# Kernel tuning notes

Measured on AMD Instinct MI355X. Metric: run time of the kernel, lower is better.

Reference implementation:

```python
import jax, jax.numpy as jnp
import numpy as np

N = 40000          # nodes
E = 640000         # edges (avg degree 16)
D_MODEL = 128
H = 8              # num_heads
DH = 16            # d_head
DFF = 512
CLAMP = 5.0
EPS = 1e-5


def setup_inputs() -> dict:
    key = jax.random.key(0)
    ks = jax.random.split(key, 10)
    s = 0.08  # weight init scale
    return {
        "feat": jax.random.normal(ks[0], (N, D_MODEL), dtype=jnp.float32),
        "src": jax.random.randint(ks[1], (E,), 0, N, dtype=jnp.int32),
        "dst": jax.random.randint(ks[2], (E,), 0, N, dtype=jnp.int32),
        "Wq": jax.random.normal(ks[3], (H * DH, D_MODEL), dtype=jnp.float32) * s,
        "Wk": jax.random.normal(ks[4], (H * DH, D_MODEL), dtype=jnp.float32) * s,
        "Wv": jax.random.normal(ks[5], (H * DH, D_MODEL), dtype=jnp.float32) * s,
        "Wo": jax.random.normal(ks[6], (D_MODEL, H * DH), dtype=jnp.float32) * s,
        "ln1_g": jnp.ones((D_MODEL,), jnp.float32),
        "ln1_b": jnp.zeros((D_MODEL,), jnp.float32),
        "W1": jax.random.normal(ks[7], (DFF, D_MODEL), dtype=jnp.float32) * s,
        "b1": jnp.zeros((DFF,), jnp.float32),
        "W2": jax.random.normal(ks[8], (D_MODEL, DFF), dtype=jnp.float32) * s,
        "b2": jnp.zeros((D_MODEL,), jnp.float32),
        "ln2_g": jnp.ones((D_MODEL,), jnp.float32),
        "ln2_b": jnp.zeros((D_MODEL,), jnp.float32),
    }


def _layer_norm(x, g, b):
    mu = jnp.mean(x, axis=-1, keepdims=True)
    var = jnp.mean(jnp.square(x - mu), axis=-1, keepdims=True)
    return (x - mu) * jax.lax.rsqrt(var + EPS) * g + b


def reference(feat, src, dst, Wq, Wk, Wv, Wo, ln1_g, ln1_b, W1, b1, W2, b2, ln2_g, ln2_b):
    n = feat.shape[0]
    # Node-level projections (equivalent to DGL's per-edge Linear on gathered feats)
    q = (feat @ Wq.T).reshape(n, H, DH)
    k = (feat @ Wk.T).reshape(n, H, DH)
    v = (feat @ Wv.T).reshape(n, H, DH)

    # Per-edge multi-head attention logits: q[dst] . k[src] / sqrt(d_head), clamped
    u = jnp.sum(q[dst] * k[src], axis=-1) / np.sqrt(DH)   # [E, H]
    u = jnp.clip(u, -CLAMP, CLAMP)

    # Ragged edge-softmax over incoming edges of each dst node
    m = jax.ops.segment_max(u, dst, num_segments=n)        # [N, H]
    e = jnp.exp(u - m[dst])                                # [E, H]
    denom = jax.ops.segment_sum(e, dst, num_segments=n)    # [N, H]
    a = e / denom[dst]                                     # [E, H]

    # Weighted V scatter-reduce back to dst nodes
    av = (a[:, :, None] * v[src]).reshape(-1, H * DH)      # [E, H*DH]
    sum_av = jax.ops.segment_sum(av, dst, num_segments=n)  # [N, H*DH]
    uh = sum_av @ Wo.T                                     # [N, d_model]

    h1 = _layer_norm(feat + uh, ln1_g, ln1_b)
    ffn = jax.nn.relu(h1 @ W1.T + b1) @ W2.T + b2
    return _layer_norm(h1 + ffn, ln2_g, ln2_b)
```

## Files before the change

### kernel.cpp

```cpp
#include <hip/hip_runtime.h>

#define DM 128
#define DFF 512
#define CLAMP_V 5.0f
#define LN_EPS 1e-5f

typedef __attribute__((ext_vector_type(8))) short bf16x8;
typedef __attribute__((ext_vector_type(4))) float f32x4;

__device__ __forceinline__ float b2f(ushort u) {
  union { uint u; float f; } x; x.u = ((uint)u) << 16; return x.f;
}
__device__ __forceinline__ ushort f2b(float f) {
  union { float f; uint u; } x; x.f = f;
  uint r = x.u + 0x7FFFu + ((x.u >> 16) & 1u);
  return (ushort)(r >> 16);
}
__device__ __forceinline__ void unpackw(uint w, float& lo, float& hi) {
  union { uint u; float f; } A, B;
  A.u = w << 16; B.u = w & 0xFFFF0000u;
  lo = A.f; hi = B.f;
}
__device__ __forceinline__ void unpack8w(uint4 w, float* o) {
  unpackw(w.x, o[0], o[1]); unpackw(w.y, o[2], o[3]);
  unpackw(w.z, o[4], o[5]); unpackw(w.w, o[6], o[7]);
}

__global__ void k_cast(const float* __restrict__ s, ushort* __restrict__ d, int n) {
  int i4 = (blockIdx.x * blockDim.x + threadIdx.x) * 4;
  if (i4 + 3 < n) {
    float4 v = *reinterpret_cast<const float4*>(s + i4);
    ushort4 o; o.x = f2b(v.x); o.y = f2b(v.y); o.z = f2b(v.z); o.w = f2b(v.w);
    *reinterpret_cast<ushort4*>(d + i4) = o;
  } else {
    for (; i4 < n; ++i4) d[i4] = f2b(s[i4]);
  }
}

__global__ void k_castw(const float* __restrict__ wq, const float* __restrict__ wk,
                        const float* __restrict__ wv, const float* __restrict__ wo,
                        const float* __restrict__ w1, const float* __restrict__ w2,
                        ushort* __restrict__ d) {
  int i4 = (blockIdx.x * blockDim.x + threadIdx.x) * 4;
  if (i4 >= 196608) return;
  const float* s; int o;
  if      (i4 < 16384)  { s = wq; o = i4; }
  else if (i4 < 32768)  { s = wk; o = i4 - 16384; }
  else if (i4 < 49152)  { s = wv; o = i4 - 32768; }
  else if (i4 < 65536)  { s = wo; o = i4 - 49152; }
  else if (i4 < 131072) { s = w1; o = i4 - 65536; }
  else                  { s = w2; o = i4 - 131072; }
  float4 v = *reinterpret_cast<const float4*>(s + o);
  ushort4 u; u.x = f2b(v.x); u.y = f2b(v.y); u.z = f2b(v.z); u.w = f2b(v.w);
  *reinterpret_cast<ushort4*>(d + i4) = u;
}

__global__ void k_count(const int* __restrict__ dst, int* __restrict__ deg, int E) {
  int e = blockIdx.x * blockDim.x + threadIdx.x;
  if (e < E) atomicAdd(&deg[dst[e]], 1);
}

#define SC_EPB 1024

__global__ __launch_bounds__(256) void k_scan1(const int* __restrict__ deg,
                                               int* __restrict__ off,
                                               int* __restrict__ bsum, int n) {
  __shared__ int sh[256];
  const int t = threadIdx.x;
  int base = blockIdx.x * SC_EPB + t * 4;
  int4 v = {0, 0, 0, 0};
  if (base + 3 < n) {
    v = *reinterpret_cast<const int4*>(deg + base);
  } else {
    if (base     < n) v.x = deg[base];
    if (base + 1 < n) v.y = deg[base + 1];
    if (base + 2 < n) v.z = deg[base + 2];
    if (base + 3 < n) v.w = deg[base + 3];
  }
  int s = v.x + v.y + v.z + v.w;
  sh[t] = s;
  __syncthreads();
  #pragma unroll
  for (int d = 1; d < 256; d <<= 1) {
    int x = 0;
    if (t >= d) x = sh[t - d];
    __syncthreads();
    sh[t] += x;
    __syncthreads();
  }
  int ex = sh[t] - s;
  if (base + 3 < n) {
    int4 o; o.x = ex; o.y = ex + v.x; o.z = ex + v.x + v.y; o.w = ex + v.x + v.y + v.z;
    *reinterpret_cast<int4*>(off + base) = o;
  } else {
    if (base     < n) off[base]     = ex;
    if (base + 1 < n) off[base + 1] = ex + v.x;
    if (base + 2 < n) off[base + 2] = ex + v.x + v.y;
    if (base + 3 < n) off[base + 3] = ex + v.x + v.y + v.z;
  }
  if (t == 255) bsum[blockIdx.x] = sh[255];
}

__global__ __launch_bounds__(256) void k_scan2(int* __restrict__ bsum, int nb) {
  __shared__ int sh[256];
  const int t = threadIdx.x;
  int v = (t < nb) ? bsum[t] : 0;
  sh[t] = v;
  __syncthreads();
  #pragma unroll
  for (int d = 1; d < 256; d <<= 1) {
    int x = 0;
    if (t >= d) x = sh[t - d];
    __syncthreads();
    sh[t] += x;
    __syncthreads();
  }
  if (t < nb) bsum[t] = sh[t] - v;
}

__global__ __launch_bounds__(256) void k_scan3(int* __restrict__ off,
                                               const int* __restrict__ bsum,
                                               int n, int E) {
  int add = bsum[blockIdx.x];
  int base = blockIdx.x * SC_EPB + threadIdx.x * 4;
  if (base + 3 < n) {
    int4 v = *reinterpret_cast<int4*>(off + base);
    v.x += add; v.y += add; v.z += add; v.w += add;
    *reinterpret_cast<int4*>(off + base) = v;
  } else {
    if (base     < n) off[base]     += add;
    if (base + 1 < n) off[base + 1] += add;
    if (base + 2 < n) off[base + 2] += add;
  }
  if (blockIdx.x == 0 && threadIdx.x == 0) off[n] = E;
}

__global__ void k_scatter(const int* __restrict__ src, const int* __restrict__ dst,
                          const int* __restrict__ off, int* __restrict__ cur,
                          int* __restrict__ csr, int E) {
  int e = blockIdx.x * blockDim.x + threadIdx.x;
  if (e < E) {
    int d = dst[e];
    int p = off[d] + atomicAdd(&cur[d], 1);
    csr[p] = src[e];
  }
}

#define BM 128
#define BN 128
#define BK 64

template<int FLAGS, bool OUTF, bool OUTB>
__global__ __launch_bounds__(256, 3) void k_mm(
    const ushort* __restrict__ A, const ushort* __restrict__ W,
    const float* __restrict__ bias, const float* __restrict__ res,
    const float* __restrict__ lng, const float* __restrict__ lnbv,
    float* __restrict__ Cf, ushort* __restrict__ Cb,
    int M, int NO, int K)
{
  __shared__ ushort As[BM * BK];
  __shared__ ushort Ws[BN * BK];
  __shared__ float lnred[(FLAGS & 8) ? 512 : 4];

  const int tid = threadIdx.x;
  const int wv = tid >> 6, ln = tid & 63;
  const int bm = blockIdx.y * BM, bn = blockIdx.x * BN;
  const int wrow = (wv >> 1) * 64, wcol = (wv & 1) * 64;

  f32x4 acc[4][4] = {};
  const int o_base = wv * 1024 + ln * 16;

  for (int k0 = 0; k0 < K; k0 += BK) {
    #pragma unroll
    for (int is = 0; is < 4; ++is) {
      int o = is * 4096 + o_base;
      int row = o >> 7;
      int c = ((o >> 4) & 7) ^ (row & 7);
      int gm = bm + row; if (gm >= M) gm = M - 1;
      const ushort* srcA = A + (size_t)gm * K + k0 + c * 8;
      __builtin_amdgcn_global_load_lds(
          (const __attribute__((address_space(1))) void*)srcA,
          (__attribute__((address_space(3))) void*)((char*)As + is * 4096 + wv * 1024),
          16, 0, 0);
      int gn = bn + row;
      const ushort* srcW = W + (size_t)gn * K + k0 + c * 8;
      __builtin_amdgcn_global_load_lds(
          (const __attribute__((address_space(1))) void*)srcW,
          (__attribute__((address_space(3))) void*)((char*)Ws + is * 4096 + wv * 1024),
          16, 0, 0);
    }
    __syncthreads();

    const char* AsB = (const char*)As;
    const char* WsB = (const char*)Ws;
    #pragma unroll
    for (int kk = 0; kk < 2; ++kk) {
      bf16x8 af[4], bf[4];
      #pragma unroll
      for (int m = 0; m < 4; ++m) {
        int r = wrow + m * 16 + (ln & 15);
        int c = kk * 4 + (ln >> 4);
        af[m] = *reinterpret_cast<const bf16x8*>(AsB + r * 128 + ((c ^ (r & 7)) << 4));
      }
      #pragma unroll
      for (int n = 0; n < 4; ++n) {
        int r = wcol + n * 16 + (ln & 15);
        int c = kk * 4 + (ln >> 4);
        bf[n] = *reinterpret_cast<const bf16x8*>(WsB + r * 128 + ((c ^ (r & 7)) << 4));
      }
      #pragma unroll
      for (int m = 0; m < 4; ++m)
        #pragma unroll
        for (int n = 0; n < 4; ++n)
          acc[m][n] = __builtin_amdgcn_mfma_f32_16x16x32_bf16(af[m], bf[n], acc[m][n], 0, 0, 0);
    }
    __syncthreads();
  }

  if constexpr ((FLAGS & 8) != 0) {
    #pragma unroll
    for (int m = 0; m < 4; ++m)
      #pragma unroll
      for (int n = 0; n < 4; ++n) {
        int gc = wcol + n * 16 + (ln & 15);
        float bsv = (FLAGS & 1) ? bias[gc] : 0.f;
        #pragma unroll
        for (int r = 0; r < 4; ++r) {
          int gr = bm + wrow + m * 16 + (ln >> 4) * 4 + r;
          float v = acc[m][n][r] + bsv;
          if (FLAGS & 2) v = fmaxf(v, 0.f);
          if (FLAGS & 4) v += res[(size_t)min(gr, M - 1) * 128 + gc];
          acc[m][n][r] = v;
        }
      }
    #pragma unroll
    for (int m = 0; m < 4; ++m)
      #pragma unroll
      for (int r = 0; r < 4; ++r) {
        float sm = acc[m][0][r] + acc[m][1][r] + acc[m][2][r] + acc[m][3][r];
        float sq = acc[m][0][r] * acc[m][0][r] + acc[m][1][r] * acc[m][1][r]
                 + acc[m][2][r] * acc[m][2][r] + acc[m][3][r] * acc[m][3][r];
        #pragma unroll
        for (int msk = 1; msk <= 8; msk <<= 1) {
          sm += __shfl_xor(sm, msk);
          sq += __shfl_xor(sq, msk);
        }
        if ((ln & 15) == 0) {
          int row = wrow + m * 16 + (ln >> 4) * 4 + r;
          lnred[row * 4 + (wv & 1) * 2]     = sm;
          lnred[row * 4 + (wv & 1) * 2 + 1] = sq;
        }
      }
    __syncthreads();
    #pragma unroll
    for (int m = 0; m < 4; ++m)
      #pragma unroll
      for (int r = 0; r < 4; ++r) {
        int row = wrow + m * 16 + (ln >> 4) * 4 + r;
        int gr = bm + row;
        float sm = lnred[row * 4] + lnred[row * 4 + 2];
        float sq = lnred[row * 4 + 1] + lnred[row * 4 + 3];
        float mu = sm * (1.f / 128.f);
        float var = fmaxf(sq * (1.f / 128.f) - mu * mu, 0.f);
        float rstd = rsqrtf(var + LN_EPS);
        if (gr < M) {
          #pragma unroll
          for (int n = 0; n < 4; ++n) {
            int gc = wcol + n * 16 + (ln & 15);
            float y = (acc[m][n][r] - mu) * rstd * lng[gc] + lnbv[gc];
            if (OUTF) Cf[(size_t)gr * 128 + gc] = y;
            if (OUTB) Cb[(size_t)gr * 128 + gc] = f2b(y);
          }
        }
      }
  } else {
    #pragma unroll
    for (int m = 0; m < 4; ++m) {
      int gr0 = bm + wrow + m * 16 + (ln >> 4) * 4;
      #pragma unroll
      for (int n = 0; n < 4; ++n) {
        int gc = bn + wcol + n * 16 + (ln & 15);
        float bsv = (FLAGS & 1) ? bias[gc] : 0.f;
        #pragma unroll
        for (int r = 0; r < 4; ++r) {
          int gr = gr0 + r;
          if (gr >= M) continue;
          float v = acc[m][n][r] + bsv;
          if (FLAGS & 2) v = fmaxf(v, 0.f);
          if (FLAGS & 4) v += res[(size_t)gr * NO + gc];
          if (OUTF) Cf[(size_t)gr * NO + gc] = v;
          if (OUTB) Cb[(size_t)gr * NO + gc] = f2b(v);
        }
      }
    }
  }
}

__global__ __launch_bounds__(256) void k_attn(
    const ushort* __restrict__ q, const ushort* __restrict__ kv,
    const int* __restrict__ off, const int* __restrict__ csr,
    ushort* __restrict__ sav, int n)
{
  int node = blockIdx.x * 4 + (threadIdx.x >> 6);
  int lane = threadIdx.x & 63;
  if (node >= n) return;
  const int g = lane >> 3, sl = lane & 7;

  const ushort* qr = q + (size_t)node * 128 + sl * 16;
  uint4 qw0 = *reinterpret_cast<const uint4*>(qr);
  uint4 qw1 = *reinterpret_cast<const uint4*>(qr + 8);
  float qv[16];
  unpack8w(qw0, qv); unpack8w(qw1, qv + 8);

  int b = off[node], e = off[node + 1];
  float m = -1e30f, s = 0.f;
  float a[16] = {};
  int nIt = (e - b + 7) >> 3;
  int idx = b + g;
  int sn = (b < e) ? csr[min(idx, e - 1)] : 0;

  for (int i = 0; i < nIt; ++i) {
    bool act = idx < e;
    const ushort* kr = kv + (size_t)sn * 256 + sl * 16;
    uint4 kw0 = *reinterpret_cast<const uint4*>(kr);
    uint4 kw1 = *reinterpret_cast<const uint4*>(kr + 8);
    uint4 vw0 = *reinterpret_cast<const uint4*>(kr + 128);
    uint4 vw1 = *reinterpret_cast<const uint4*>(kr + 136);
    idx += 8;
    if (i + 1 < nIt) sn = csr[min(idx, e - 1)];

    float kk[16];
    unpack8w(kw0, kk); unpack8w(kw1, kk + 8);
    float p = 0.f;
    #pragma unroll
    for (int j = 0; j < 16; ++j) p = fmaf(qv[j], kk[j], p);
    float u = fminf(fmaxf(p * 0.25f, -CLAMP_V), CLAMP_V);
    if (act) {
      float mn = fmaxf(m, u);
      float f = __expf(m - mn);
      float w = __expf(u - mn);
      s = s * f + w;
      float vvv[16];
      unpack8w(vw0, vvv); unpack8w(vw1, vvv + 8);
      #pragma unroll
      for (int j = 0; j < 16; ++j) a[j] = a[j] * f + w * vvv[j];
      m = mn;
    }
  }

  #pragma unroll
  for (int msk = 8; msk <= 32; msk <<= 1) {
    float mo = __shfl_xor(m, msk);
    float so = __shfl_xor(s, msk);
    float ao[16];
    #pragma unroll
    for (int j = 0; j < 16; ++j) ao[j] = __shfl_xor(a[j], msk);
    float mn = fmaxf(m, mo);
    float f1 = __expf(m - mn), f2 = __expf(mo - mn);
    s = s * f1 + so * f2;
    #pragma unroll
    for (int j = 0; j < 16; ++j) a[j] = a[j] * f1 + ao[j] * f2;
    m = mn;
  }

  float inv = (s > 0.f) ? 1.f / s : 0.f;
  if (g == 0) {
    uint w[8];
    #pragma unroll
    for (int j = 0; j < 8; ++j)
      w[j] = (uint)f2b(a[2 * j] * inv) | ((uint)f2b(a[2 * j + 1] * inv) << 16);
    ushort* outp = sav + (size_t)node * 128 + sl * 16;
    uint4 o0 = {w[0], w[1], w[2], w[3]};
    uint4 o1 = {w[4], w[5], w[6], w[7]};
    *reinterpret_cast<uint4*>(outp) = o0;
    *reinterpret_cast<uint4*>(outp + 8) = o1;
  }
}

extern "C" void kernel_launch(void* const* d_in, const int* in_sizes, int n_in,
                              void* d_out, int out_size, void* d_ws, size_t ws_size,
                              hipStream_t stream)
{
  const float* feat = (const float*)d_in[0];
  const int*   src  = (const int*)d_in[1];
  const int*   dst  = (const int*)d_in[2];
  const float* Wq   = (const float*)d_in[3];
  const float* Wk   = (const float*)d_in[4];
  const float* Wv   = (const float*)d_in[5];
  const float* Wo   = (const float*)d_in[6];
  const float* ln1g = (const float*)d_in[7];
  const float* ln1b = (const float*)d_in[8];
  const float* W1   = (const float*)d_in[9];
  const float* b1   = (const float*)d_in[10];
  const float* W2   = (const float*)d_in[11];
  const float* b2   = (const float*)d_in[12];
  const float* ln2g = (const float*)d_in[13];
  const float* ln2b = (const float*)d_in[14];
  float* out = (float*)d_out;

  const int N = in_sizes[0] / DM;
  const int E = in_sizes[1];
  const size_t NB = (size_t)N;

  char* wsb = (char*)d_ws;
  ushort* q_bf    = (ushort*)wsb;
  ushort* kv_bf   = (ushort*)(wsb + NB * 256);
  ushort* sav_bf  = (ushort*)(wsb + NB * 768);
  ushort* mid_bf  = (ushort*)wsb;
  float*  h1      = (float*)(wsb + NB * 1024);
  ushort* h1b     = (ushort*)(wsb + NB * 1536);
  ushort* feat_bf = (ushort*)(wsb + NB * 1792);
  ushort* wbf     = (ushort*)(wsb + NB * 2048);
  ushort* wqkv_bf = wbf;
  ushort* wo_bf   = wbf + 49152;
  ushort* w1_bf   = wbf + 65536;
  ushort* w2_bf   = wbf + 131072;
  int* ib  = (int*)(wbf + 196608);
  int* deg = ib;
  int* cur = ib + N;
  int* off = ib + 2 * N;
  int* csr = ib + 3 * N + 1;
  int* bsum = csr + E;

  hipMemsetAsync(deg, 0, 2 * (size_t)N * sizeof(int), stream);

  int nf = N * DM;
  k_cast<<<(nf / 4 + 255) / 256, 256, 0, stream>>>(feat, feat_bf, nf);
  k_castw<<<192, 256, 0, stream>>>(Wq, Wk, Wv, Wo, W1, W2, wbf);

  int eb = (E + 255) / 256;
  int nbk = (N + SC_EPB - 1) / SC_EPB;
  k_count<<<eb, 256, 0, stream>>>(dst, deg, E);
  k_scan1<<<nbk, 256, 0, stream>>>(deg, off, bsum, N);
  k_scan2<<<1, 256, 0, stream>>>(bsum, nbk);
  k_scan3<<<nbk, 256, 0, stream>>>(off, bsum, N, E);
  k_scatter<<<eb, 256, 0, stream>>>(src, dst, off, cur, csr, E);

  const int gy = (N + BM - 1) / BM;
  int nb4 = (N + 3) / 4;

  k_mm<0, false, true><<<dim3(1, gy), 256, 0, stream>>>(
      feat_bf, wqkv_bf, nullptr, nullptr, nullptr, nullptr, nullptr, q_bf, N, DM, DM);
  k_mm<0, false, true><<<dim3(2, gy), 256, 0, stream>>>(
      feat_bf, wqkv_bf + 16384, nullptr, nullptr, nullptr, nullptr, nullptr, kv_bf, N, 256, DM);

  k_attn<<<nb4, 256, 0, stream>>>(q_bf, kv_bf, off, csr, sav_bf, N);

  k_mm<4 | 8, true, true><<<dim3(1, gy), 256, 0, stream>>>(
      sav_bf, wo_bf, nullptr, feat, ln1g, ln1b, h1, h1b, N, DM, DM);

  k_mm<1 | 2, false, true><<<dim3(4, gy), 256, 0, stream>>>(
      h1b, w1_bf, b1, nullptr, nullptr, nullptr, nullptr, mid_bf, N, DFF, DM);

  k_mm<1 | 4 | 8, true, false><<<dim3(1, gy), 256, 0, stream>>>(
      mid_bf, w2_bf, b2, h1, ln2g, ln2b, out, nullptr, N, DM, DFF);
}
```

Before: 203.5 us.

## Add persistent weight-stationary GEMMs, double-buffer K loop, drop online softmax max

Adds a persistent 512-thread GEMM (k_mmS) for the K=128 projections. It keeps one 128x128 weight tile resident in LDS, walks several row tiles per block, and double-buffers the A tiles. It also fuses the Q and KV projections into one launch. The K=512 FFN-down GEMM now double-buffers its K loop at lower occupancy. The attention kernel drops the running max and uses the fixed clamp bound 5 as the softmax shift, removing rescale exps and branches. That shift is exact in math because logits are clamped, but it loses the per-node max normalization.

```diff
diff --git a/kernel.cpp b/kernel.cpp
--- a/kernel.cpp
+++ b/kernel.cpp
@@ -146,56 +146,240 @@
   }
 }
 
+template<int FLAGS, bool QKVSPLIT, bool OUTF, bool OUTB>
+__global__ __launch_bounds__(512, 1) void k_mmS(
+    const ushort* __restrict__ A, const ushort* __restrict__ W,
+    const float* __restrict__ bias, const float* __restrict__ res,
+    const float* __restrict__ lng, const float* __restrict__ lnbv,
+    float* __restrict__ Cf, ushort* __restrict__ Cb, ushort* __restrict__ Cb2,
+    int M, int ldc)
+{
+  __shared__ ushort Bs[128 * 128];
+  __shared__ ushort As[2][128 * 128];
+  __shared__ float lnred[(FLAGS & 8) ? 1024 : 4];
+
+  const int tid = threadIdx.x;
+  const int wv = tid >> 6, ln = tid & 63;
+  const int bnb = blockIdx.x;
+  const int wrow = (wv >> 2) * 64, wcol = (wv & 3) * 32;
+  const int o_base = wv * 1024 + ln * 16;
+
+  const int nT = (M + 127) >> 7;
+  const int T = (nT + gridDim.y - 1) / gridDim.y;
+  const int t0 = blockIdx.y * T;
+  const int t1 = min(t0 + T, nT);
+  if (t0 >= nT) return;
+
+  #pragma unroll
+  for (int is = 0; is < 4; ++is) {
+    int o = is * 8192 + o_base;
+    int row = o >> 8;
+    int c = ((o >> 4) & 15) ^ (row & 15);
+    const ushort* s = W + (size_t)(bnb * 128 + row) * 128 + c * 8;
+    __builtin_amdgcn_global_load_lds(
+        (const __attribute__((address_space(1))) void*)s,
+        (__attribute__((address_space(3))) void*)((char*)Bs + is * 8192 + wv * 1024),
+        16, 0, 0);
+  }
+  {
+    #pragma unroll
+    for (int is = 0; is < 4; ++is) {
+      int o = is * 8192 + o_base;
+      int row = o >> 8;
+      int c = ((o >> 4) & 15) ^ (row & 15);
+      int gr = min(t0 * 128 + row, M - 1);
+      const ushort* s = A + (size_t)gr * 128 + c * 8;
+      __builtin_amdgcn_global_load_lds(
+          (const __attribute__((address_space(1))) void*)s,
+          (__attribute__((address_space(3))) void*)((char*)As[0] + is * 8192 + wv * 1024),
+          16, 0, 0);
+    }
+  }
+  __syncthreads();
+
+  int buf = 0;
+  for (int t = t0; t < t1; ++t) {
+    if (t + 1 < t1) {
+      #pragma unroll
+      for (int is = 0; is < 4; ++is) {
+        int o = is * 8192 + o_base;
+        int row = o >> 8;
+        int c = ((o >> 4) & 15) ^ (row & 15);
+        int gr = min((t + 1) * 128 + row, M - 1);
+        const ushort* s = A + (size_t)gr * 128 + c * 8;
+        __builtin_amdgcn_global_load_lds(
+            (const __attribute__((address_space(1))) void*)s,
+            (__attribute__((address_space(3))) void*)((char*)As[buf ^ 1] + is * 8192 + wv * 1024),
+            16, 0, 0);
+      }
+    }
+
+    f32x4 acc[4][2] = {};
+    const char* AsB = (const char*)As[buf];
+    const char* BsB = (const char*)Bs;
+    #pragma unroll
+    for (int kk = 0; kk < 4; ++kk) {
+      bf16x8 af[4], bfr[2];
+      #pragma unroll
+      for (int m = 0; m < 4; ++m) {
+        int r = wrow + m * 16 + (ln & 15);
+        int c = kk * 4 + (ln >> 4);
+        af[m] = *reinterpret_cast<const bf16x8*>(AsB + r * 256 + ((c ^ (r & 15)) << 4));
+      }
+      #pragma unroll
+      for (int n = 0; n < 2; ++n) {
+        int r = wcol + n * 16 + (ln & 15);
+        int c = kk * 4 + (ln >> 4);
+        bfr[n] = *reinterpret_cast<const bf16x8*>(BsB + r * 256 + ((c ^ (r & 15)) << 4));
+      }
+      #pragma unroll
+      for (int m = 0; m < 4; ++m)
+        #pragma unroll
+        for (int n = 0; n < 2; ++n)
+          acc[m][n] = __builtin_amdgcn_mfma_f32_16x16x32_bf16(af[m], bfr[n], acc[m][n], 0, 0, 0);
+    }
+
+    const int mbase = t * 128;
+    if constexpr ((FLAGS & 8) != 0) {
+      #pragma unroll
+      for (int m = 0; m < 4; ++m)
+        #pragma unroll
+        for (int n = 0; n < 2; ++n) {
+          int gc = wcol + n * 16 + (ln & 15);
+          #pragma unroll
+          for (int r = 0; r < 4; ++r) {
+            int gr = mbase + wrow + m * 16 + (ln >> 4) * 4 + r;
+            float v = acc[m][n][r];
+            if (FLAGS & 1) v += bias[gc];
+            if (FLAGS & 2) v = fmaxf(v, 0.f);
+            if (FLAGS & 4) v += res[(size_t)min(gr, M - 1) * 128 + gc];
+            acc[m][n][r] = v;
+          }
+        }
+      #pragma unroll
+      for (int m = 0; m < 4; ++m)
+        #pragma unroll
+        for (int r = 0; r < 4; ++r) {
+          float sm = acc[m][0][r] + acc[m][1][r];
+          float sq = acc[m][0][r] * acc[m][0][r] + acc[m][1][r] * acc[m][1][r];
+          #pragma unroll
+          for (int msk = 1; msk <= 8; msk <<= 1) {
+            sm += __shfl_xor(sm, msk);
+            sq += __shfl_xor(sq, msk);
+          }
+          if ((ln & 15) == 0) {
+            int row = wrow + m * 16 + (ln >> 4) * 4 + r;
+            lnred[row * 8 + (wv & 3) * 2]     = sm;
+            lnred[row * 8 + (wv & 3) * 2 + 1] = sq;
+          }
+        }
+      __syncthreads();
+      #pragma unroll
+      for (int m = 0; m < 4; ++m)
+        #pragma unroll
+        for (int r = 0; r < 4; ++r) {
+          int row = wrow + m * 16 + (ln >> 4) * 4 + r;
+          int gr = mbase + row;
+          float sm = lnred[row * 8] + lnred[row * 8 + 2] + lnred[row * 8 + 4] + lnred[row * 8 + 6];
+          float sq = lnred[row * 8 + 1] + lnred[row * 8 + 3] + lnred[row * 8 + 5] + lnred[row * 8 + 7];
+          float mu = sm * (1.f / 128.f);
+          float var = fmaxf(sq * (1.f / 128.f) - mu * mu, 0.f);
+          float rstd = rsqrtf(var + LN_EPS);
+          if (gr < M) {
+            #pragma unroll
+            for (int n = 0; n < 2; ++n) {
+              int gc = wcol + n * 16 + (ln & 15);
+              float y = (acc[m][n][r] - mu) * rstd * lng[gc] + lnbv[gc];
+              if (OUTF) Cf[(size_t)gr * 128 + gc] = y;
+              if (OUTB) Cb[(size_t)gr * 128 + gc] = f2b(y);
+            }
+          }
+        }
+    } else {
+      #pragma unroll
+      for (int m = 0; m < 4; ++m) {
+        int gr0 = mbase + wrow + m * 16 + (ln >> 4) * 4;
+        #pragma unroll
+        for (int n = 0; n < 2; ++n) {
+          int gcl = wcol + n * 16 + (ln & 15);
+          float bsv = (FLAGS & 1) ? bias[bnb * 128 + gcl] : 0.f;
+          #pragma unroll
+          for (int r = 0; r < 4; ++r) {
+            int gr = gr0 + r;
+            if (gr >= M) continue;
+            float v = acc[m][n][r] + bsv;
+            if (FLAGS & 2) v = fmaxf(v, 0.f);
+            if (QKVSPLIT) {
+              if (bnb == 0) Cb[(size_t)gr * 128 + gcl] = f2b(v);
+              else          Cb2[(size_t)gr * 256 + (bnb - 1) * 128 + gcl] = f2b(v);
+            } else {
+              if (OUTF) Cf[(size_t)gr * ldc + bnb * 128 + gcl] = v;
+              if (OUTB) Cb[(size_t)gr * ldc + bnb * 128 + gcl] = f2b(v);
+            }
+          }
+        }
+      }
+    }
+    __syncthreads();
+    buf ^= 1;
+  }
+}
+
 #define BM 128
 #define BN 128
 #define BK 64
 
 template<int FLAGS, bool OUTF, bool OUTB>
-__global__ __launch_bounds__(256, 3) void k_mm(
+__global__ __launch_bounds__(256, 2) void k_mm2(
     const ushort* __restrict__ A, const ushort* __restrict__ W,
     const float* __restrict__ bias, const float* __restrict__ res,
     const float* __restrict__ lng, const float* __restrict__ lnbv,
     float* __restrict__ Cf, ushort* __restrict__ Cb,
     int M, int NO, int K)
 {
-  __shared__ ushort As[BM * BK];
-  __shared__ ushort Ws[BN * BK];
+  __shared__ ushort As[2][BM * BK];
+  __shared__ ushort Ws[2][BN * BK];
   __shared__ float lnred[(FLAGS & 8) ? 512 : 4];
 
   const int tid = threadIdx.x;
   const int wv = tid >> 6, ln = tid & 63;
   const int bm = blockIdx.y * BM, bn = blockIdx.x * BN;
   const int wrow = (wv >> 1) * 64, wcol = (wv & 1) * 64;
-
-  f32x4 acc[4][4] = {};
   const int o_base = wv * 1024 + ln * 16;
 
-  for (int k0 = 0; k0 < K; k0 += BK) {
+  auto STG = [&](int kidx, int b) {
     #pragma unroll
     for (int is = 0; is < 4; ++is) {
       int o = is * 4096 + o_base;
       int row = o >> 7;
       int c = ((o >> 4) & 7) ^ (row & 7);
-      int gm = bm + row; if (gm >= M) gm = M - 1;
-      const ushort* srcA = A + (size_t)gm * K + k0 + c * 8;
+      int gm = min(bm + row, M - 1);
+      const ushort* sA = A + (size_t)gm * K + kidx * BK + c * 8;
       __builtin_amdgcn_global_load_lds(
-          (const __attribute__((address_space(1))) void*)srcA,
-          (__attribute__((address_space(3))) void*)((char*)As + is * 4096 + wv * 1024),
+          (const __attribute__((address_space(1))) void*)sA,
+          (__attribute__((address_space(3))) void*)((char*)As[b] + is * 4096 + wv * 1024),
           16, 0, 0);
       int gn = bn + row;
-      const ushort* srcW = W + (size_t)gn * K + k0 + c * 8;
+      const ushort* sW = W + (size_t)gn * K + kidx * BK + c * 8;
       __builtin_amdgcn_global_load_lds(
-          (const __attribute__((address_space(1))) void*)srcW,
-          (__attribute__((address_space(3))) void*)((char*)Ws + is * 4096 + wv * 1024),
+          (const __attribute__((address_space(1))) void*)sW,
+          (__attribute__((address_space(3))) void*)((char*)Ws[b] + is * 4096 + wv * 1024),
           16, 0, 0);
     }
-    __syncthreads();
-
-    const char* AsB = (const char*)As;
-    const char* WsB = (const char*)Ws;
+  };
+
+  f32x4 acc[4][4] = {};
+  const int KT = K >> 6;
+  STG(0, 0);
+  __syncthreads();
+  int buf = 0;
+  for (int i = 0; i < KT; ++i) {
+    if (i + 1 < KT) STG(i + 1, buf ^ 1);
+    const char* AsB = (const char*)As[buf];
+    const char* WsB = (const char*)Ws[buf];
     #pragma unroll
     for (int kk = 0; kk < 2; ++kk) {
-      bf16x8 af[4], bf[4];
+      bf16x8 af[4], bfr[4];
       #pragma unroll
       for (int m = 0; m < 4; ++m) {
         int r = wrow + m * 16 + (ln & 15);
@@ -206,15 +390,16 @@
       for (int n = 0; n < 4; ++n) {
         int r = wcol + n * 16 + (ln & 15);
         int c = kk * 4 + (ln >> 4);
-        bf[n] = *reinterpret_cast<const bf16x8*>(WsB + r * 128 + ((c ^ (r & 7)) << 4));
+        bfr[n] = *reinterpret_cast<const bf16x8*>(WsB + r * 128 + ((c ^ (r & 7)) << 4));
       }
       #pragma unroll
       for (int m = 0; m < 4; ++m)
         #pragma unroll
         for (int n = 0; n < 4; ++n)
-          acc[m][n] = __builtin_amdgcn_mfma_f32_16x16x32_bf16(af[m], bf[n], acc[m][n], 0, 0, 0);
+          acc[m][n] = __builtin_amdgcn_mfma_f32_16x16x32_bf16(af[m], bfr[n], acc[m][n], 0, 0, 0);
     }
     __syncthreads();
+    buf ^= 1;
   }
 
   if constexpr ((FLAGS & 8) != 0) {
@@ -313,7 +498,7 @@
   unpack8w(qw0, qv); unpack8w(qw1, qv + 8);
 
   int b = off[node], e = off[node + 1];
-  float m = -1e30f, s = 0.f;
+  float s = 0.f;
   float a[16] = {};
   int nIt = (e - b + 7) >> 3;
   int idx = b + g;
@@ -335,32 +520,20 @@
     #pragma unroll
     for (int j = 0; j < 16; ++j) p = fmaf(qv[j], kk[j], p);
     float u = fminf(fmaxf(p * 0.25f, -CLAMP_V), CLAMP_V);
-    if (act) {
-      float mn = fmaxf(m, u);
-      float f = __expf(m - mn);
-      float w = __expf(u - mn);
-      s = s * f + w;
-      float vvv[16];
-      unpack8w(vw0, vvv); unpack8w(vw1, vvv + 8);
-      #pragma unroll
-      for (int j = 0; j < 16; ++j) a[j] = a[j] * f + w * vvv[j];
-      m = mn;
-    }
+    float w = __expf(u - CLAMP_V);
+    w = act ? w : 0.f;
+    s += w;
+    float vvv[16];
+    unpack8w(vw0, vvv); unpack8w(vw1, vvv + 8);
+    #pragma unroll
+    for (int j = 0; j < 16; ++j) a[j] = fmaf(w, vvv[j], a[j]);
   }
 
   #pragma unroll
   for (int msk = 8; msk <= 32; msk <<= 1) {
-    float mo = __shfl_xor(m, msk);
-    float so = __shfl_xor(s, msk);
-    float ao[16];
-    #pragma unroll
-    for (int j = 0; j < 16; ++j) ao[j] = __shfl_xor(a[j], msk);
-    float mn = fmaxf(m, mo);
-    float f1 = __expf(m - mn), f2 = __expf(mo - mn);
-    s = s * f1 + so * f2;
-    #pragma unroll
-    for (int j = 0; j < 16; ++j) a[j] = a[j] * f1 + ao[j] * f2;
-    m = mn;
+    s += __shfl_xor(s, msk);
+    #pragma unroll
+    for (int j = 0; j < 16; ++j) a[j] += __shfl_xor(a[j], msk);
   }
 
   float inv = (s > 0.f) ? 1.f / s : 0.f;
@@ -436,22 +609,31 @@
   k_scan3<<<nbk, 256, 0, stream>>>(off, bsum, N, E);
   k_scatter<<<eb, 256, 0, stream>>>(src, dst, off, cur, csr, E);
 
-  const int gy = (N + BM - 1) / BM;
   int nb4 = (N + 3) / 4;
-
-  k_mm<0, false, true><<<dim3(1, gy), 256, 0, stream>>>(
-      feat_bf, wqkv_bf, nullptr, nullptr, nullptr, nullptr, nullptr, q_bf, N, DM, DM);
-  k_mm<0, false, true><<<dim3(2, gy), 256, 0, stream>>>(
-      feat_bf, wqkv_bf + 16384, nullptr, nullptr, nullptr, nullptr, nullptr, kv_bf, N, 256, DM);
+  const int nT = (N + 127) / 128;
+
+  {
+    int S = (nT + 3) / 4;
+    k_mmS<0, true, false, true><<<dim3(3, S), 512, 0, stream>>>(
+        feat_bf, wqkv_bf, nullptr, nullptr, nullptr, nullptr,
+        nullptr, q_bf, kv_bf, N, 0);
+  }
 
   k_attn<<<nb4, 256, 0, stream>>>(q_bf, kv_bf, off, csr, sav_bf, N);
 
-  k_mm<4 | 8, true, true><<<dim3(1, gy), 256, 0, stream>>>(
-      sav_bf, wo_bf, nullptr, feat, ln1g, ln1b, h1, h1b, N, DM, DM);
-
-  k_mm<1 | 2, false, true><<<dim3(4, gy), 256, 0, stream>>>(
-      h1b, w1_bf, b1, nullptr, nullptr, nullptr, nullptr, mid_bf, N, DFF, DM);
-
-  k_mm<1 | 4 | 8, true, false><<<dim3(1, gy), 256, 0, stream>>>(
+  {
+    int S = (nT + 1) / 2;
+    k_mmS<4 | 8, false, true, true><<<dim3(1, S), 512, 0, stream>>>(
+        sav_bf, wo_bf, nullptr, feat, ln1g, ln1b, h1, h1b, nullptr, N, 128);
+  }
+
+  {
+    int S = (nT + 4) / 5;
+    k_mmS<1 | 2, false, false, true><<<dim3(4, S), 512, 0, stream>>>(
+        h1b, w1_bf, b1, nullptr, nullptr, nullptr,
+        nullptr, mid_bf, nullptr, N, DFF);
+  }
+
+  k_mm2<1 | 4 | 8, true, false><<<dim3(1, nT), 256, 0, stream>>>(
       mid_bf, w2_bf, b2, h1, ln2g, ln2b, out, nullptr, N, DM, DFF);
 }
```

Result: no change. 199.9 us (-1.8%).

## Drop LDS staging in GEMMs, fixed-max softmax, and merge small launches

Applied to the files above, without the earlier changes.

The GEMM kernel now loads MFMA fragments straight from global memory instead of staging them through LDS, which removes the barriers but relies on cache for reuse. The Q and KV projections become one launch that writes two outputs. The attention kernel drops the online-softmax running max and uses the clamp bound as a fixed shift, which is exact in math because logits are clamped to 5. It also replaces the max-rescale reduction with plain sums. The two cast kernels are merged, and scan2 is folded into scan3 through a per-block wave reduction.

```diff
diff --git a/kernel.cpp b/kernel.cpp
--- a/kernel.cpp
+++ b/kernel.cpp
@@ -26,22 +26,20 @@
   unpackw(w.z, o[4], o[5]); unpackw(w.w, o[6], o[7]);
 }
 
-__global__ void k_cast(const float* __restrict__ s, ushort* __restrict__ d, int n) {
-  int i4 = (blockIdx.x * blockDim.x + threadIdx.x) * 4;
-  if (i4 + 3 < n) {
-    float4 v = *reinterpret_cast<const float4*>(s + i4);
+__global__ void k_castall(const float* __restrict__ feat,
+                          const float* __restrict__ wq, const float* __restrict__ wk,
+                          const float* __restrict__ wv, const float* __restrict__ wo,
+                          const float* __restrict__ w1, const float* __restrict__ w2,
+                          ushort* __restrict__ feat_bf, ushort* __restrict__ wbf,
+                          int nf4) {
+  int i = blockIdx.x * blockDim.x + threadIdx.x;
+  if (i < nf4) {
+    float4 v = *reinterpret_cast<const float4*>(feat + i * 4);
     ushort4 o; o.x = f2b(v.x); o.y = f2b(v.y); o.z = f2b(v.z); o.w = f2b(v.w);
-    *reinterpret_cast<ushort4*>(d + i4) = o;
-  } else {
-    for (; i4 < n; ++i4) d[i4] = f2b(s[i4]);
-  }
-}
-
-__global__ void k_castw(const float* __restrict__ wq, const float* __restrict__ wk,
-                        const float* __restrict__ wv, const float* __restrict__ wo,
-                        const float* __restrict__ w1, const float* __restrict__ w2,
-                        ushort* __restrict__ d) {
-  int i4 = (blockIdx.x * blockDim.x + threadIdx.x) * 4;
+    *reinterpret_cast<ushort4*>(feat_bf + i * 4) = o;
+    return;
+  }
+  int i4 = (i - nf4) * 4;
   if (i4 >= 196608) return;
   const float* s; int o;
   if      (i4 < 16384)  { s = wq; o = i4; }
@@ -52,7 +50,7 @@
   else                  { s = w2; o = i4 - 131072; }
   float4 v = *reinterpret_cast<const float4*>(s + o);
   ushort4 u; u.x = f2b(v.x); u.y = f2b(v.y); u.z = f2b(v.z); u.w = f2b(v.w);
-  *reinterpret_cast<ushort4*>(d + i4) = u;
+  *reinterpret_cast<ushort4*>(wbf + i4) = u;
 }
 
 __global__ void k_count(const int* __restrict__ dst, int* __restrict__ deg, int E) {
@@ -101,28 +99,20 @@
   if (t == 255) bsum[blockIdx.x] = sh[255];
 }
 
-__global__ __launch_bounds__(256) void k_scan2(int* __restrict__ bsum, int nb) {
-  __shared__ int sh[256];
-  const int t = threadIdx.x;
-  int v = (t < nb) ? bsum[t] : 0;
-  sh[t] = v;
-  __syncthreads();
-  #pragma unroll
-  for (int d = 1; d < 256; d <<= 1) {
-    int x = 0;
-    if (t >= d) x = sh[t - d];
-    __syncthreads();
-    sh[t] += x;
-    __syncthreads();
-  }
-  if (t < nb) bsum[t] = sh[t] - v;
-}
-
 __global__ __launch_bounds__(256) void k_scan3(int* __restrict__ off,
                                                const int* __restrict__ bsum,
-                                               int n, int E) {
-  int add = bsum[blockIdx.x];
-  int base = blockIdx.x * SC_EPB + threadIdx.x * 4;
+                                               int nbk, int n, int E) {
+  __shared__ int sadd;
+  const int t = threadIdx.x;
+  if (t < 64) {
+    int v = (t < nbk && t < (int)blockIdx.x) ? bsum[t] : 0;
+    #pragma unroll
+    for (int msk = 1; msk < 64; msk <<= 1) v += __shfl_xor(v, msk);
+    if (t == 0) sadd = v;
+  }
+  __syncthreads();
+  int add = sadd;
+  int base = blockIdx.x * SC_EPB + t * 4;
   if (base + 3 < n) {
     int4 v = *reinterpret_cast<int4*>(off + base);
     v.x += add; v.y += add; v.z += add; v.w += add;
@@ -132,7 +122,7 @@
     if (base + 1 < n) off[base + 1] += add;
     if (base + 2 < n) off[base + 2] += add;
   }
-  if (blockIdx.x == 0 && threadIdx.x == 0) off[n] = E;
+  if (blockIdx.x == 0 && t == 0) off[n] = E;
 }
 
 __global__ void k_scatter(const int* __restrict__ src, const int* __restrict__ dst,
@@ -146,75 +136,48 @@
   }
 }
 
-#define BM 128
-#define BN 128
-#define BK 64
-
-template<int FLAGS, bool OUTF, bool OUTB>
-__global__ __launch_bounds__(256, 3) void k_mm(
+template<int FLAGS, bool QKVSPLIT, bool OUTF, bool OUTB>
+__global__ __launch_bounds__(256) void k_mmR(
     const ushort* __restrict__ A, const ushort* __restrict__ W,
     const float* __restrict__ bias, const float* __restrict__ res,
     const float* __restrict__ lng, const float* __restrict__ lnbv,
-    float* __restrict__ Cf, ushort* __restrict__ Cb,
-    int M, int NO, int K)
+    float* __restrict__ Cf, ushort* __restrict__ Cb, ushort* __restrict__ Cb2,
+    int M, int K, int NO)
 {
-  __shared__ ushort As[BM * BK];
-  __shared__ ushort Ws[BN * BK];
   __shared__ float lnred[(FLAGS & 8) ? 512 : 4];
-
   const int tid = threadIdx.x;
   const int wv = tid >> 6, ln = tid & 63;
-  const int bm = blockIdx.y * BM, bn = blockIdx.x * BN;
+  const int bnb = blockIdx.x;
+  const int mbase = blockIdx.y * 128;
   const int wrow = (wv >> 1) * 64, wcol = (wv & 1) * 64;
+  const int lr = ln & 15;
+  const int lc = (ln >> 4) * 8;
+
+  const ushort* Ab[4];
+  const ushort* Wb[4];
+  #pragma unroll
+  for (int m = 0; m < 4; ++m) {
+    int gr = min(mbase + wrow + m * 16 + lr, M - 1);
+    Ab[m] = A + (size_t)gr * K + lc;
+  }
+  #pragma unroll
+  for (int n = 0; n < 4; ++n) {
+    int gc = bnb * 128 + wcol + n * 16 + lr;
+    Wb[n] = W + (size_t)gc * K + lc;
+  }
 
   f32x4 acc[4][4] = {};
-  const int o_base = wv * 1024 + ln * 16;
-
-  for (int k0 = 0; k0 < K; k0 += BK) {
-    #pragma unroll
-    for (int is = 0; is < 4; ++is) {
-      int o = is * 4096 + o_base;
-      int row = o >> 7;
-      int c = ((o >> 4) & 7) ^ (row & 7);
-      int gm = bm + row; if (gm >= M) gm = M - 1;
-      const ushort* srcA = A + (size_t)gm * K + k0 + c * 8;
-      __builtin_amdgcn_global_load_lds(
-          (const __attribute__((address_space(1))) void*)srcA,
-          (__attribute__((address_space(3))) void*)((char*)As + is * 4096 + wv * 1024),
-          16, 0, 0);
-      int gn = bn + row;
-      const ushort* srcW = W + (size_t)gn * K + k0 + c * 8;
-      __builtin_amdgcn_global_load_lds(
-          (const __attribute__((address_space(1))) void*)srcW,
-          (__attribute__((address_space(3))) void*)((char*)Ws + is * 4096 + wv * 1024),
-          16, 0, 0);
-    }
-    __syncthreads();
-
-    const char* AsB = (const char*)As;
-    const char* WsB = (const char*)Ws;
-    #pragma unroll
-    for (int kk = 0; kk < 2; ++kk) {
-      bf16x8 af[4], bf[4];
+  for (int k0 = 0; k0 < K; k0 += 32) {
+    bf16x8 af[4], bf[4];
+    #pragma unroll
+    for (int m = 0; m < 4; ++m) af[m] = *reinterpret_cast<const bf16x8*>(Ab[m] + k0);
+    #pragma unroll
+    for (int n = 0; n < 4; ++n) bf[n] = *reinterpret_cast<const bf16x8*>(Wb[n] + k0);
+    #pragma unroll
+    for (int m = 0; m < 4; ++m)
       #pragma unroll
-      for (int m = 0; m < 4; ++m) {
-        int r = wrow + m * 16 + (ln & 15);
-        int c = kk * 4 + (ln >> 4);
-        af[m] = *reinterpret_cast<const bf16x8*>(AsB + r * 128 + ((c ^ (r & 7)) << 4));
-      }
-      #pragma unroll
-      for (int n = 0; n < 4; ++n) {
-        int r = wcol + n * 16 + (ln & 15);
-        int c = kk * 4 + (ln >> 4);
-        bf[n] = *reinterpret_cast<const bf16x8*>(WsB + r * 128 + ((c ^ (r & 7)) << 4));
-      }
-      #pragma unroll
-      for (int m = 0; m < 4; ++m)
-        #pragma unroll
-        for (int n = 0; n < 4; ++n)
-          acc[m][n] = __builtin_amdgcn_mfma_f32_16x16x32_bf16(af[m], bf[n], acc[m][n], 0, 0, 0);
-    }
-    __syncthreads();
+      for (int n = 0; n < 4; ++n)
+        acc[m][n] = __builtin_amdgcn_mfma_f32_16x16x32_bf16(af[m], bf[n], acc[m][n], 0, 0, 0);
   }
 
   if constexpr ((FLAGS & 8) != 0) {
@@ -222,11 +185,11 @@
     for (int m = 0; m < 4; ++m)
       #pragma unroll
       for (int n = 0; n < 4; ++n) {
-        int gc = wcol + n * 16 + (ln & 15);
+        int gc = wcol + n * 16 + lr;
         float bsv = (FLAGS & 1) ? bias[gc] : 0.f;
         #pragma unroll
         for (int r = 0; r < 4; ++r) {
-          int gr = bm + wrow + m * 16 + (ln >> 4) * 4 + r;
+          int gr = mbase + wrow + m * 16 + (ln >> 4) * 4 + r;
           float v = acc[m][n][r] + bsv;
           if (FLAGS & 2) v = fmaxf(v, 0.f);
           if (FLAGS & 4) v += res[(size_t)min(gr, M - 1) * 128 + gc];
@@ -245,7 +208,7 @@
           sm += __shfl_xor(sm, msk);
           sq += __shfl_xor(sq, msk);
         }
-        if ((ln & 15) == 0) {
+        if (lr == 0) {
           int row = wrow + m * 16 + (ln >> 4) * 4 + r;
           lnred[row * 4 + (wv & 1) * 2]     = sm;
           lnred[row * 4 + (wv & 1) * 2 + 1] = sq;
@@ -257,7 +220,7 @@
       #pragma unroll
       for (int r = 0; r < 4; ++r) {
         int row = wrow + m * 16 + (ln >> 4) * 4 + r;
-        int gr = bm + row;
+        int gr = mbase + row;
         float sm = lnred[row * 4] + lnred[row * 4 + 2];
         float sq = lnred[row * 4 + 1] + lnred[row * 4 + 3];
         float mu = sm * (1.f / 128.f);
@@ -266,7 +229,7 @@
         if (gr < M) {
           #pragma unroll
           for (int n = 0; n < 4; ++n) {
-            int gc = wcol + n * 16 + (ln & 15);
+            int gc = wcol + n * 16 + lr;
             float y = (acc[m][n][r] - mu) * rstd * lng[gc] + lnbv[gc];
             if (OUTF) Cf[(size_t)gr * 128 + gc] = y;
             if (OUTB) Cb[(size_t)gr * 128 + gc] = f2b(y);
@@ -276,20 +239,25 @@
   } else {
     #pragma unroll
     for (int m = 0; m < 4; ++m) {
-      int gr0 = bm + wrow + m * 16 + (ln >> 4) * 4;
+      int gr0 = mbase + wrow + m * 16 + (ln >> 4) * 4;
       #pragma unroll
       for (int n = 0; n < 4; ++n) {
-        int gc = bn + wcol + n * 16 + (ln & 15);
-        float bsv = (FLAGS & 1) ? bias[gc] : 0.f;
+        int gcl = wcol + n * 16 + lr;
+        float bsv = (FLAGS & 1) ? bias[bnb * 128 + gcl] : 0.f;
         #pragma unroll
         for (int r = 0; r < 4; ++r) {
           int gr = gr0 + r;
           if (gr >= M) continue;
           float v = acc[m][n][r] + bsv;
           if (FLAGS & 2) v = fmaxf(v, 0.f);
-          if (FLAGS & 4) v += res[(size_t)gr * NO + gc];
-          if (OUTF) Cf[(size_t)gr * NO + gc] = v;
-          if (OUTB) Cb[(size_t)gr * NO + gc] = f2b(v);
+          if (FLAGS & 4) v += res[(size_t)gr * NO + bnb * 128 + gcl];
+          if (QKVSPLIT) {
+            if (bnb == 0) Cb[(size_t)gr * 128 + gcl] = f2b(v);
+            else          Cb2[(size_t)gr * 256 + (bnb - 1) * 128 + gcl] = f2b(v);
+          } else {
+            if (OUTF) Cf[(size_t)gr * NO + bnb * 128 + gcl] = v;
+            if (OUTB) Cb[(size_t)gr * NO + bnb * 128 + gcl] = f2b(v);
+          }
         }
       }
     }
@@ -313,7 +281,7 @@
   unpack8w(qw0, qv); unpack8w(qw1, qv + 8);
 
   int b = off[node], e = off[node + 1];
-  float m = -1e30f, s = 0.f;
+  float s = 0.f;
   float a[16] = {};
   int nIt = (e - b + 7) >> 3;
   int idx = b + g;
@@ -335,32 +303,20 @@
     #pragma unroll
     for (int j = 0; j < 16; ++j) p = fmaf(qv[j], kk[j], p);
     float u = fminf(fmaxf(p * 0.25f, -CLAMP_V), CLAMP_V);
-    if (act) {
-      float mn = fmaxf(m, u);
-      float f = __expf(m - mn);
-      float w = __expf(u - mn);
-      s = s * f + w;
-      float vvv[16];
-      unpack8w(vw0, vvv); unpack8w(vw1, vvv + 8);
-      #pragma unroll
-      for (int j = 0; j < 16; ++j) a[j] = a[j] * f + w * vvv[j];
-      m = mn;
-    }
+    float w = __expf(u - CLAMP_V);
+    w = act ? w : 0.f;
+    s += w;
+    float vvv[16];
+    unpack8w(vw0, vvv); unpack8w(vw1, vvv + 8);
+    #pragma unroll
+    for (int j = 0; j < 16; ++j) a[j] = fmaf(w, vvv[j], a[j]);
   }
 
   #pragma unroll
   for (int msk = 8; msk <= 32; msk <<= 1) {
-    float mo = __shfl_xor(m, msk);
-    float so = __shfl_xor(s, msk);
-    float ao[16];
-    #pragma unroll
-    for (int j = 0; j < 16; ++j) ao[j] = __shfl_xor(a[j], msk);
-    float mn = fmaxf(m, mo);
-    float f1 = __expf(m - mn), f2 = __expf(mo - mn);
-    s = s * f1 + so * f2;
-    #pragma unroll
-    for (int j = 0; j < 16; ++j) a[j] = a[j] * f1 + ao[j] * f2;
-    m = mn;
+    s += __shfl_xor(s, msk);
+    #pragma unroll
+    for (int j = 0; j < 16; ++j) a[j] += __shfl_xor(a[j], msk);
   }
 
   float inv = (s > 0.f) ? 1.f / s : 0.f;
@@ -424,34 +380,33 @@
 
   hipMemsetAsync(deg, 0, 2 * (size_t)N * sizeof(int), stream);
 
-  int nf = N * DM;
-  k_cast<<<(nf / 4 + 255) / 256, 256, 0, stream>>>(feat, feat_bf, nf);
-  k_castw<<<192, 256, 0, stream>>>(Wq, Wk, Wv, Wo, W1, W2, wbf);
+  int nf4 = N * DM / 4;
+  k_castall<<<(nf4 + 49152 + 255) / 256, 256, 0, stream>>>(
+      feat, Wq, Wk, Wv, Wo, W1, W2, feat_bf, wbf, nf4);
 
   int eb = (E + 255) / 256;
   int nbk = (N + SC_EPB - 1) / SC_EPB;
   k_count<<<eb, 256, 0, stream>>>(dst, deg, E);
   k_scan1<<<nbk, 256, 0, stream>>>(deg, off, bsum, N);
-  k_scan2<<<1, 256, 0, stream>>>(bsum, nbk);
-  k_scan3<<<nbk, 256, 0, stream>>>(off, bsum, N, E);
+  k_scan3<<<nbk, 256, 0, stream>>>(off, bsum, nbk, N, E);
   k_scatter<<<eb, 256, 0, stream>>>(src, dst, off, cur, csr, E);
 
-  const int gy = (N + BM - 1) / BM;
   int nb4 = (N + 3) / 4;
-
-  k_mm<0, false, true><<<dim3(1, gy), 256, 0, stream>>>(
-      feat_bf, wqkv_bf, nullptr, nullptr, nullptr, nullptr, nullptr, q_bf, N, DM, DM);
-  k_mm<0, false, true><<<dim3(2, gy), 256, 0, stream>>>(
-      feat_bf, wqkv_bf + 16384, nullptr, nullptr, nullptr, nullptr, nullptr, kv_bf, N, 256, DM);
+  const int nT = (N + 127) / 128;
+
+  k_mmR<0, true, false, true><<<dim3(3, nT), 256, 0, stream>>>(
+      feat_bf, wqkv_bf, nullptr, nullptr, nullptr, nullptr,
+      nullptr, q_bf, kv_bf, N, DM, 384);
 
   k_attn<<<nb4, 256, 0, stream>>>(q_bf, kv_bf, off, csr, sav_bf, N);
 
-  k_mm<4 | 8, true, true><<<dim3(1, gy), 256, 0, stream>>>(
-      sav_bf, wo_bf, nullptr, feat, ln1g, ln1b, h1, h1b, N, DM, DM);
-
-  k_mm<1 | 2, false, true><<<dim3(4, gy), 256, 0, stream>>>(
-      h1b, w1_bf, b1, nullptr, nullptr, nullptr, nullptr, mid_bf, N, DFF, DM);
-
-  k_mm<1 | 4 | 8, true, false><<<dim3(1, gy), 256, 0, stream>>>(
-      mid_bf, w2_bf, b2, h1, ln2g, ln2b, out, nullptr, N, DM, DFF);
-}
+  k_mmR<4 | 8, false, true, true><<<dim3(1, nT), 256, 0, stream>>>(
+      sav_bf, wo_bf, nullptr, feat, ln1g, ln1b, h1, h1b, nullptr, N, DM, DM);
+
+  k_mmR<1 | 2, false, false, true><<<dim3(4, nT), 256, 0, stream>>>(
+      h1b, w1_bf, b1, nullptr, nullptr, nullptr,
+      nullptr, mid_bf, nullptr, N, DM, DFF);
+
+  k_mmR<1 | 4 | 8, false, true, false><<<dim3(1, nT), 256, 0, stream>>>(
+      mid_bf, w2_bf, b2, h1, ln2g, ln2b, out, nullptr, nullptr, N, DFF, DM);
+}
```

After: 237.4 us. 1.17x slower.
